# Kernel tuning notes

Measured on AMD Instinct MI355X. Metric: run time of the kernel, lower is better.

Reference implementation:

```python
import jax, jax.numpy as jnp
import numpy as np

# config constants
D = 1024       # main_dim
HD = 64        # attn_head_dim
NH = 16        # attention heads = D // HD
H = 16         # main_head_num (routing heads)
KH = 8         # main_key_head_num
KC = 2         # main_key_repeat_num (KH*KC == H)
N = 128        # block_size
E = 4096       # total_layer_expert_num
RE = 4         # aux_router_expert_num
DE = 4         # selected experts per router
ET = RE * DE   # 16
B, S = 1, 2048
T = B * S
BC = T // N    # 16
EPS = 1e-5
THETA = 10000.0


def rmsnorm(x, w):
    return x * jax.lax.rsqrt(jnp.mean(x * x, axis=-1, keepdims=True) + EPS) * w


def l2norm(x):
    n = jnp.sqrt(jnp.sum(x * x, axis=-1, keepdims=True))
    return x / jnp.maximum(n, EPS)


def rope(x):
    # x: (b, h, s, a); matches RotaryEmb: y1 = x1*cos + x2*sin, y2 = -x1*sin + x2*cos
    a = x.shape[-1]
    s = x.shape[2]
    inv_freq = (1.0 / THETA) ** (jnp.arange(0, a, 2, dtype=jnp.float32) / a)
    freqs = jnp.arange(s, dtype=jnp.float32)[:, None] * inv_freq[None, :]  # (s, a/2)
    cos, sin = jnp.cos(freqs), jnp.sin(freqs)
    x1, x2 = jnp.split(x, 2, axis=-1)
    return jnp.concatenate([x1 * cos + x2 * sin, -x1 * sin + x2 * cos], axis=-1)


def setup_inputs() -> dict:
    key = jax.random.key(0)
    ks = jax.random.split(key, 10)
    return {
        "x_input": jax.random.normal(ks[0], (B, S, D), jnp.float32),
        "indices": jax.random.randint(ks[1], (BC, RE, DE), 0, E),
        "scores": jax.random.normal(ks[2], (T, ET, H), jnp.float32),
        "attn_w": jax.random.normal(ks[3], (D, 3 * D), jnp.float32) * 0.02,
        "attn_out_w": jax.random.normal(ks[4], (D, D), jnp.float32) * 0.02,
        "attn_norm_w": jnp.ones((D,), jnp.float32),
        "ffn_norm_w": jnp.ones((D,), jnp.float32),
        "ffn_experts": jax.random.normal(ks[5], (3, E, D, 1), jnp.float32) * 0.02,
        "keys": jax.random.normal(ks[6], (KH, D, E), jnp.float32) * 0.02,
        "head_probs": jnp.full((1, RE, E, H), 1.0 / H, jnp.float32)
                      + 0.01 * jax.random.normal(ks[7], (1, RE, E, H), jnp.float32),
        "score_probs": jnp.full((2, 1, RE, E, H), 0.5, jnp.float32)
                       + 0.01 * jax.random.normal(ks[8], (2, 1, RE, E, H), jnp.float32),
    }


def reference(x_input, indices, scores, attn_w, attn_out_w, attn_norm_w,
              ffn_norm_w, ffn_experts, keys, head_probs, score_probs):
    # --- attention block ---
    x = rmsnorm(x_input, attn_norm_w)
    qkv = x @ attn_w                                   # (b, s, 3d)
    xq, xk, xv = jnp.split(qkv, 3, axis=-1)

    def heads(t):  # 'b s (h a) -> b h s a'
        return t.reshape(B, S, NH, HD).transpose(0, 2, 1, 3)

    xq, xk, xv = heads(xq), heads(xk), heads(xv)
    xq, xk = l2norm(xq), l2norm(xk)                    # qk_norm
    xq, xk = rope(xq), rope(xk)

    att = jnp.einsum('bhqa,bhka->bhqk', xq, xk) / np.sqrt(HD)
    causal = jnp.tril(jnp.ones((S, S), bool))
    att = jnp.where(causal, att, -jnp.inf)
    att = jax.nn.softmax(att, axis=-1)
    x_attn = jnp.einsum('bhqk,bhka->bhqa', att, xv)
    x_attn = x_attn.transpose(0, 2, 1, 3).reshape(B, S, D)
    x_attn_output = x_attn @ attn_out_w
    x_ffn_input = x_attn_output + x_input

    # --- product-key routing ---
    x_ffn = rmsnorm(x_ffn_input, ffn_norm_w)
    xf = x_ffn.reshape(T, D)

    keys_r = jnp.repeat(keys, KC, axis=0)              # (H, D, E)
    ms = jnp.einsum('td,hde->teh', xf, keys_r)         # (T, E, H)

    idx_flat = indices.reshape(BC, ET)                 # (BC, ET)
    idx_tok = jnp.repeat(idx_flat, N, axis=0)          # (T, ET), token t -> block t//N
    main_g = jnp.take_along_axis(ms, idx_tok[:, :, None], axis=1)  # (T, ET, H)

    r_idx = jnp.arange(RE)[None, :, None]
    sp = score_probs[:, 0]                             # (2, RE, E, H)
    sp_g = sp[:, r_idx, indices]                       # (2, BC, RE, DE, H)
    sp_g = jnp.repeat(sp_g.reshape(2, BC, ET, H), N, axis=1)       # (2, T, ET, H)

    comb = jax.nn.sigmoid(sp_g[0] * main_g + sp_g[1] * scores)     # (T, ET, H)

    hp_g = head_probs[0][r_idx, indices]               # (BC, RE, DE, H)
    hp_g = jnp.repeat(hp_g.reshape(BC, ET, H), N, axis=0)          # (T, ET, H)

    w = jnp.sum(comb * hp_g, axis=-1)                  # (T, ET) pair weights

    # --- grouped GEMM over tiny (d -> expert_dim -> d) experts, SwiGLU ---
    Wg = ffn_experts[:, idx_tok]                       # (3, T, ET, D, expert_dim)
    h0 = jnp.einsum('td,tedk->tek', xf, Wg[0])
    h1 = jnp.einsum('td,tedk->tek', xf, Wg[1])
    act = jax.nn.silu(h0) * h1 * w[:, :, None]         # (T, ET, expert_dim)
    out = jnp.einsum('tek,tedk->td', act, Wg[2])       # sum over selected experts

    return out.reshape(B, S, D) + x_ffn_input
```

## Files before the change

### kernel.cpp

```cpp
#include <hip/hip_runtime.h>
#include <hip/hip_bf16.h>
#include <math.h>

#define D_   1024
#define HD_  64
#define NH_  16
#define H_   16
#define KH_  8
#define NT_  128
#define E_   4096
#define RE_  4
#define DE_  4
#define ET_  16
#define S_   2048
#define T_   2048
#define BC_  16
#define EPS_ 1e-5f

typedef short s16x8 __attribute__((ext_vector_type(8)));
typedef float f32x4 __attribute__((ext_vector_type(4)));

__device__ __forceinline__ unsigned short f2bf(float f) {
    union { float f; unsigned int u; } v; v.f = f;
    unsigned int r = (v.u + 0x7fffu + ((v.u >> 16) & 1u)) >> 16;
    return (unsigned short)r;
}

#define GLOAD16(gp, lp) __builtin_amdgcn_global_load_lds(                      \
    (__attribute__((address_space(1))) void*)(gp),                             \
    (__attribute__((address_space(3))) void*)(lp), 16, 0, 0)

__global__ __launch_bounds__(256) void preprocess_kernel(
    const float* __restrict__ x, const float* __restrict__ attn_norm_w,
    unsigned short* __restrict__ xnb,
    const float* __restrict__ attn_w, unsigned short* __restrict__ wqkvT,
    const float* __restrict__ attn_out_w, unsigned short* __restrict__ woutT,
    const float* __restrict__ keys, const int* __restrict__ indices,
    unsigned short* __restrict__ tmpT)
{
    __shared__ float tile[32][33];
    __shared__ float sred[4];
    __shared__ float rowbuf[E_];
    int bid = blockIdx.x, tid = threadIdx.x;

    if (bid < 2048) {
        int row = bid;
        float4 v = ((const float4*)(x + (size_t)row * D_))[tid];
        float ss = v.x*v.x + v.y*v.y + v.z*v.z + v.w*v.w;
#pragma unroll
        for (int off = 32; off > 0; off >>= 1) ss += __shfl_xor(ss, off);
        if ((tid & 63) == 0) sred[tid >> 6] = ss;
        __syncthreads();
        float tot = sred[0] + sred[1] + sred[2] + sred[3];
        float scale = rsqrtf(tot * (1.0f / D_) + EPS_);
        float4 wv = ((const float4*)attn_norm_w)[tid];
        ushort4 o;
        o.x = f2bf(v.x * scale * wv.x);
        o.y = f2bf(v.y * scale * wv.y);
        o.z = f2bf(v.z * scale * wv.z);
        o.w = f2bf(v.w * scale * wv.w);
        *(ushort4*)(xnb + (size_t)row * D_ + tid * 4) = o;
    } else if (bid < 6144) {
        const float* src; unsigned short* dst; int R, Ncols, bx, by;
        if (bid < 5120) {
            int cid = bid - 2048;
            src = attn_w; dst = wqkvT; R = D_; Ncols = 3 * D_;
            bx = (cid % 96) * 32; by = (cid / 96) * 32;
        } else {
            int cid = bid - 5120;
            src = attn_out_w; dst = woutT; R = D_; Ncols = D_;
            bx = (cid & 31) * 32; by = (cid >> 5) * 32;
        }
        int tx = tid & 31, ty = tid >> 5;
#pragma unroll
        for (int rr = 0; rr < 32; rr += 8)
            tile[ty + rr][tx] = src[(size_t)(by + ty + rr) * Ncols + bx + tx];
        __syncthreads();
#pragma unroll
        for (int rr = 0; rr < 32; rr += 8)
            dst[(size_t)(bx + ty + rr) * R + by + tx] = f2bf(tile[tx][ty + rr]);
    } else {
        int id = bid - 6144;
        int kh = id >> 10;
        int d  = id & (D_ - 1);
        const float* rowp = keys + ((size_t)kh * D_ + d) * E_;
#pragma unroll
        for (int pass = 0; pass < 4; pass++)
            ((float4*)rowbuf)[tid + pass * 256] =
                ((const float4*)rowp)[tid + pass * 256];
        __syncthreads();
        int idx = indices[tid];
        tmpT[((size_t)kh * D_ + d) * 256 + tid] = f2bf(rowbuf[idx]);
    }
}

__global__ __launch_bounds__(256) void transpose_keys_kernel(
    const unsigned short* __restrict__ tmpT, unsigned short* __restrict__ kgath)
{
    __shared__ unsigned short tile[32][34];
    int p0 = blockIdx.x * 32;
    int d0 = blockIdx.y * 32;
    int kh = blockIdx.z;
    int tx = threadIdx.x & 31, ty = threadIdx.x >> 5;
#pragma unroll
    for (int rr = 0; rr < 32; rr += 8)
        tile[ty + rr][tx] = tmpT[((size_t)kh * D_ + d0 + ty + rr) * 256 + p0 + tx];
    __syncthreads();
#pragma unroll
    for (int rr = 0; rr < 32; rr += 8) {
        int p = p0 + ty + rr;
        int n = (p >> 4) * 128 + (p & 15) * 8 + kh;
        kgath[(size_t)n * D_ + d0 + tx] = tile[tx][ty + rr];
    }
}

__global__ __launch_bounds__(256) void rmsnorm_dual_kernel(
    const float* __restrict__ x, const float* __restrict__ w,
    float* __restrict__ out, unsigned short* __restrict__ outb)
{
    int row = blockIdx.x, tid = threadIdx.x;
    __shared__ float sred[4];
    float4 v = ((const float4*)(x + (size_t)row * D_))[tid];
    float ss = v.x*v.x + v.y*v.y + v.z*v.z + v.w*v.w;
#pragma unroll
    for (int off = 32; off > 0; off >>= 1) ss += __shfl_xor(ss, off);
    if ((tid & 63) == 0) sred[tid >> 6] = ss;
    __syncthreads();
    float tot = sred[0] + sred[1] + sred[2] + sred[3];
    float scale = rsqrtf(tot * (1.0f / D_) + EPS_);
    float4 wv = ((const float4*)w)[tid];
    float4 o;
    o.x = v.x * scale * wv.x;
    o.y = v.y * scale * wv.y;
    o.z = v.z * scale * wv.z;
    o.w = v.w * scale * wv.w;
    ((float4*)(out + (size_t)row * D_))[tid] = o;
    ushort4 ob;
    ob.x = f2bf(o.x); ob.y = f2bf(o.y); ob.z = f2bf(o.z); ob.w = f2bf(o.w);
    *(ushort4*)(outb + (size_t)row * D_ + tid * 4) = ob;
}

template <int WITH_RES>
__global__ __launch_bounds__(256) void mfma_gemm_kernel(
    const unsigned short* __restrict__ A, const unsigned short* __restrict__ Bt,
    const float* __restrict__ res, float* __restrict__ C,
    int M, int N, int K)
{
    __shared__ __align__(16) short As[128][32];
    __shared__ __align__(16) short Bs[128][32];
    int tid = threadIdx.x;
    int wave = tid >> 6, lane = tid & 63;
    int ml = lane & 15, q = lane >> 4;
    int wr = wave >> 1, wc = wave & 1;
    int bm = blockIdx.y * 128, bn = blockIdx.x * 128;
    int srow = tid >> 2;
    int scol = (tid & 3) * 8;

    f32x4 acc[4][4];
#pragma unroll
    for (int i = 0; i < 4; i++)
#pragma unroll
        for (int j = 0; j < 4; j++) acc[i][j] = (f32x4){0.f, 0.f, 0.f, 0.f};

    const unsigned short* Ap = A  + (size_t)(bm + srow) * K + scol;
    const unsigned short* Bp = Bt + (size_t)(bn + srow) * K + scol;
    short* ldsA0 = &As[wave * 16][0];
    short* ldsA1 = &As[64 + wave * 16][0];
    short* ldsB0 = &Bs[wave * 16][0];
    short* ldsB1 = &Bs[64 + wave * 16][0];

    for (int k0 = 0; k0 < K; k0 += 32) {
        __syncthreads();
        GLOAD16(Ap + k0, ldsA0);
        GLOAD16(Ap + (size_t)64 * K + k0, ldsA1);
        GLOAD16(Bp + k0, ldsB0);
        GLOAD16(Bp + (size_t)64 * K + k0, ldsB1);
        __syncthreads();

        s16x8 af[4], bf[4];
#pragma unroll
        for (int i = 0; i < 4; i++)
            af[i] = *(const s16x8*)(&As[wr * 64 + i * 16 + ml][q * 8]);
#pragma unroll
        for (int j = 0; j < 4; j++)
            bf[j] = *(const s16x8*)(&Bs[wc * 64 + j * 16 + ml][q * 8]);
#pragma unroll
        for (int i = 0; i < 4; i++)
#pragma unroll
            for (int j = 0; j < 4; j++)
                acc[i][j] = __builtin_amdgcn_mfma_f32_16x16x32_bf16(
                    af[i], bf[j], acc[i][j], 0, 0, 0);
    }

#pragma unroll
    for (int i = 0; i < 4; i++) {
#pragma unroll
        for (int j = 0; j < 4; j++) {
            int col = bn + wc * 64 + j * 16 + ml;
#pragma unroll
            for (int r = 0; r < 4; r++) {
                int row = bm + wr * 64 + i * 16 + q * 4 + r;
                float v = acc[i][j][r];
                if (WITH_RES) v += res[(size_t)row * N + col];
                C[(size_t)row * N + col] = v;
            }
        }
    }
}

__global__ __launch_bounds__(256) void mfma_gemm_qkv_kernel(
    const unsigned short* __restrict__ A, const unsigned short* __restrict__ Bt,
    unsigned short* __restrict__ qh, unsigned short* __restrict__ khb,
    unsigned short* __restrict__ vhT)
{
    const int K = D_;
    __shared__ __align__(16) short As[128][32];
    __shared__ __align__(16) short Bs[128][32];
    int tid = threadIdx.x;
    int wave = tid >> 6, lane = tid & 63;
    int ml = lane & 15, q = lane >> 4;
    int wr = wave >> 1, wc = wave & 1;
    int bm = blockIdx.y * 128, bn = blockIdx.x * 128;
    int srow = tid >> 2;
    int scol = (tid & 3) * 8;

    f32x4 acc[4][4];
#pragma unroll
    for (int i = 0; i < 4; i++)
#pragma unroll
        for (int j = 0; j < 4; j++) acc[i][j] = (f32x4){0.f, 0.f, 0.f, 0.f};

    const unsigned short* Ap = A  + (size_t)(bm + srow) * K + scol;
    const unsigned short* Bp = Bt + (size_t)(bn + srow) * K + scol;
    short* ldsA0 = &As[wave * 16][0];
    short* ldsA1 = &As[64 + wave * 16][0];
    short* ldsB0 = &Bs[wave * 16][0];
    short* ldsB1 = &Bs[64 + wave * 16][0];

    for (int k0 = 0; k0 < K; k0 += 32) {
        __syncthreads();
        GLOAD16(Ap + k0, ldsA0);
        GLOAD16(Ap + (size_t)64 * K + k0, ldsA1);
        GLOAD16(Bp + k0, ldsB0);
        GLOAD16(Bp + (size_t)64 * K + k0, ldsB1);
        __syncthreads();

        s16x8 af[4], bf[4];
#pragma unroll
        for (int i = 0; i < 4; i++)
            af[i] = *(const s16x8*)(&As[wr * 64 + i * 16 + ml][q * 8]);
#pragma unroll
        for (int j = 0; j < 4; j++)
            bf[j] = *(const s16x8*)(&Bs[wc * 64 + j * 16 + ml][q * 8]);
#pragma unroll
        for (int i = 0; i < 4; i++)
#pragma unroll
            for (int j = 0; j < 4; j++)
                acc[i][j] = __builtin_amdgcn_mfma_f32_16x16x32_bf16(
                    af[i], bf[j], acc[i][j], 0, 0, 0);
    }

    int sel = blockIdx.x >> 3;
    int h = ((blockIdx.x & 7) << 1) + wc;
    float qscale = (sel == 0) ? 0.125f : 1.0f;
    float if0 = exp2f((float)ml * (-13.287712379549449f / 32.0f));
    float if1 = exp2f((float)(16 + ml) * (-13.287712379549449f / 32.0f));

#pragma unroll
    for (int i = 0; i < 4; i++) {
#pragma unroll
        for (int r = 0; r < 4; r++) {
            int row = bm + wr * 64 + i * 16 + q * 4 + r;
            float v0 = acc[i][0][r], v1 = acc[i][1][r];
            float v2 = acc[i][2][r], v3 = acc[i][3][r];
            if (sel < 2) {
                float ss = v0*v0 + v1*v1 + v2*v2 + v3*v3;
#pragma unroll
                for (int off = 1; off < 16; off <<= 1)
                    ss += __shfl_xor(ss, off);
                float inv = qscale / fmaxf(sqrtf(ss), EPS_);
                v0 *= inv; v1 *= inv; v2 *= inv; v3 *= inv;
                float sn0, cs0, sn1, cs1;
                sincosf((float)row * if0, &sn0, &cs0);
                sincosf((float)row * if1, &sn1, &cs1);
                float o0 = v0 * cs0 + v2 * sn0;
                float o2 = v2 * cs0 - v0 * sn0;
                float o1 = v1 * cs1 + v3 * sn1;
                float o3 = v3 * cs1 - v1 * sn1;
                v0 = o0; v1 = o1; v2 = o2; v3 = o3;
                unsigned short* dst = (sel == 0) ? qh : khb;
                size_t base = ((size_t)h * S_ + row) * HD_;
                dst[base +      ml] = f2bf(v0);
                dst[base + 16 + ml] = f2bf(v1);
                dst[base + 32 + ml] = f2bf(v2);
                dst[base + 48 + ml] = f2bf(v3);
            } else {
                size_t base = ((size_t)h * HD_ + ml) * S_ + row;
                vhT[base            ] = f2bf(v0);
                vhT[base + 16 * S_  ] = f2bf(v1);
                vhT[base + 32 * S_  ] = f2bf(v2);
                vhT[base + 48 * S_  ] = f2bf(v3);
            }
        }
    }
}

#define FS 72
__global__ __launch_bounds__(256) void flash_attn_mfma_kernel(
    const unsigned short* __restrict__ qh, const unsigned short* __restrict__ khb,
    const unsigned short* __restrict__ vhT, unsigned short* __restrict__ aob)
{
    __shared__ __align__(16) short Ks[2][64][FS];
    __shared__ __align__(16) short Vs[2][64][FS];
    __shared__ __align__(16) short Ps[4][16][FS];
    int b = blockIdx.x;
    int xcd = b & 7, j = b >> 3;
    int h = 2 * xcd + (j & 1);
    int pp = (j >> 1) & 15;
    int t = (j >> 5) ? (31 - pp) : pp;
    int tid = threadIdx.x;
    int wq = tid >> 6;
    int lane = tid & 63;
    int ml = lane & 15, quad = lane >> 4;
    int srow = tid >> 2;
    int sc = (tid & 3) * 16;
    const unsigned short* Qb = qh  + (size_t)h * S_ * HD_;
    const unsigned short* Kb = khb + (size_t)h * S_ * HD_;
    const unsigned short* Vt = vhT + (size_t)h * HD_ * S_;

    int q0 = t * 64;
    int qrow = q0 + wq * 16 + ml;
    s16x8 aq0 = *(const s16x8*)(Qb + (size_t)qrow * HD_ + quad * 8);
    s16x8 aq1 = *(const s16x8*)(Qb + (size_t)qrow * HD_ + 32 + quad * 8);

    float ps[4];
    f32x4 o[4];
#pragma unroll
    for (int r = 0; r < 4; r++) ps[r] = 0.f;
#pragma unroll
    for (int nb = 0; nb < 4; nb++) o[nb] = (f32x4){0.f, 0.f, 0.f, 0.f};

    int4 kr0, kr1, vr0, vr1;
    {
        const unsigned short* kp = Kb + (size_t)srow * HD_ + sc;
        kr0 = *(const int4*)kp; kr1 = *(const int4*)(kp + 8);
        const unsigned short* vp = Vt + (size_t)srow * S_ + sc;
        vr0 = *(const int4*)vp; vr1 = *(const int4*)(vp + 8);
        *(int4*)(&Ks[0][srow][sc]) = kr0; *(int4*)(&Ks[0][srow][sc + 8]) = kr1;
        *(int4*)(&Vs[0][srow][sc]) = vr0; *(int4*)(&Vs[0][srow][sc + 8]) = vr1;
    }

    for (int kt = 0; kt <= t; kt++) {
        int k0 = kt * 64;
        int cur = kt & 1;
        if (kt < t) {
            const unsigned short* kp = Kb + (size_t)(k0 + 64 + srow) * HD_ + sc;
            kr0 = *(const int4*)kp; kr1 = *(const int4*)(kp + 8);
            const unsigned short* vp = Vt + (size_t)srow * S_ + k0 + 64 + sc;
            vr0 = *(const int4*)vp; vr1 = *(const int4*)(vp + 8);
        }
        __syncthreads();

        f32x4 s[4];
#pragma unroll
        for (int nb = 0; nb < 4; nb++) s[nb] = (f32x4){0.f, 0.f, 0.f, 0.f};
        __builtin_amdgcn_s_setprio(1);
#pragma unroll
        for (int nb = 0; nb < 4; nb++) {
            s16x8 b0 = *(const s16x8*)(&Ks[cur][nb * 16 + ml][quad * 8]);
            s16x8 b1 = *(const s16x8*)(&Ks[cur][nb * 16 + ml][32 + quad * 8]);
            s[nb] = __builtin_amdgcn_mfma_f32_16x16x32_bf16(aq0, b0, s[nb], 0, 0, 0);
            s[nb] = __builtin_amdgcn_mfma_f32_16x16x32_bf16(aq1, b1, s[nb], 0, 0, 0);
        }
        __builtin_amdgcn_s_setprio(0);

#pragma unroll
        for (int nb = 0; nb < 4; nb++)
#pragma unroll
            for (int r = 0; r < 4; r++) {
                float pe = __expf(s[nb][r]);
                if (kt == t && (nb * 16 + ml) > (wq * 16 + quad * 4 + r))
                    pe = 0.f;
                ps[r] += pe;
                Ps[wq][quad * 4 + r][nb * 16 + ml] = (short)f2bf(pe);
            }

        s16x8 ap0 = *(const s16x8*)(&Ps[wq][ml][quad * 8]);
        s16x8 ap1 = *(const s16x8*)(&Ps[wq][ml][32 + quad * 8]);
        __builtin_amdgcn_s_setprio(1);
#pragma unroll
        for (int nb = 0; nb < 4; nb++) {
            s16x8 b0 = *(const s16x8*)(&Vs[cur][nb * 16 + ml][quad * 8]);
            s16x8 b1 = *(const s16x8*)(&Vs[cur][nb * 16 + ml][32 + quad * 8]);
            o[nb] = __builtin_amdgcn_mfma_f32_16x16x32_bf16(ap0, b0, o[nb], 0, 0, 0);
            o[nb] = __builtin_amdgcn_mfma_f32_16x16x32_bf16(ap1, b1, o[nb], 0, 0, 0);
        }
        __builtin_amdgcn_s_setprio(0);

        if (kt < t) {
            *(int4*)(&Ks[cur ^ 1][srow][sc])     = kr0;
            *(int4*)(&Ks[cur ^ 1][srow][sc + 8]) = kr1;
            *(int4*)(&Vs[cur ^ 1][srow][sc])     = vr0;
            *(int4*)(&Vs[cur ^ 1][srow][sc + 8]) = vr1;
        }
    }

#pragma unroll
    for (int r = 0; r < 4; r++) {
        float l = ps[r];
#pragma unroll
        for (int off = 1; off < 16; off <<= 1)
            l += __shfl_xor(l, off);
        float inv = 1.0f / l;
        int row = q0 + wq * 16 + quad * 4 + r;
#pragma unroll
        for (int nb = 0; nb < 4; nb++)
            aob[(size_t)row * D_ + h * HD_ + nb * 16 + ml] =
                f2bf(o[nb][r] * inv);
    }
}

__global__ __launch_bounds__(256) void score_gemm_kernel(
    const unsigned short* __restrict__ xfb, const unsigned short* __restrict__ kgath,
    float* __restrict__ msbufp)
{
    __shared__ __align__(16) short As[128][32];
    __shared__ __align__(16) short Bs[128][32];
    int c  = blockIdx.x >> 3;
    int sk = blockIdx.x & 7;
    const unsigned short* A  = xfb   + (size_t)c * 128 * D_ + sk * 128;
    const unsigned short* Bt = kgath + (size_t)c * 128 * D_ + sk * 128;
    int tid = threadIdx.x;
    int wave = tid >> 6, lane = tid & 63;
    int ml = lane & 15, q = lane >> 4;
    int wr = wave >> 1, wc = wave & 1;
    int srow = tid >> 2;
    int scol = (tid & 3) * 8;

    f32x4 acc[4][4];
#pragma unroll
    for (int i = 0; i < 4; i++)
#pragma unroll
        for (int j = 0; j < 4; j++) acc[i][j] = (f32x4){0.f, 0.f, 0.f, 0.f};

    const unsigned short* Ap = A  + (size_t)srow * D_ + scol;
    const unsigned short* Bp = Bt + (size_t)srow * D_ + scol;
    short* ldsA0 = &As[wave * 16][0];
    short* ldsA1 = &As[64 + wave * 16][0];
    short* ldsB0 = &Bs[wave * 16][0];
    short* ldsB1 = &Bs[64 + wave * 16][0];

    for (int k0 = 0; k0 < 128; k0 += 32) {
        __syncthreads();
        GLOAD16(Ap + k0, ldsA0);
        GLOAD16(Ap + (size_t)64 * D_ + k0, ldsA1);
        GLOAD16(Bp + k0, ldsB0);
        GLOAD16(Bp + (size_t)64 * D_ + k0, ldsB1);
        __syncthreads();

        s16x8 af[4], bf[4];
#pragma unroll
        for (int i = 0; i < 4; i++)
            af[i] = *(const s16x8*)(&As[wr * 64 + i * 16 + ml][q * 8]);
#pragma unroll
        for (int j = 0; j < 4; j++)
            bf[j] = *(const s16x8*)(&Bs[wc * 64 + j * 16 + ml][q * 8]);
#pragma unroll
        for (int i = 0; i < 4; i++)
#pragma unroll
            for (int j = 0; j < 4; j++)
                acc[i][j] = __builtin_amdgcn_mfma_f32_16x16x32_bf16(
                    af[i], bf[j], acc[i][j], 0, 0, 0);
    }

    float* out = msbufp + (size_t)blockIdx.x * 128 * 128;
#pragma unroll
    for (int i = 0; i < 4; i++)
#pragma unroll
        for (int j = 0; j < 4; j++) {
            int col = wc * 64 + j * 16 + ml;
#pragma unroll
            for (int r = 0; r < 4; r++) {
                int row = wr * 64 + i * 16 + q * 4 + r;
                out[(size_t)row * 128 + col] = acc[i][j][r];
            }
        }
}

__global__ __launch_bounds__(256) void moe_kernel(
    const float* __restrict__ xf, const float* __restrict__ xfi,
    const int* __restrict__ indices, const float* __restrict__ msbufp,
    const float* __restrict__ scores,
    const float* __restrict__ score_probs, const float* __restrict__ head_probs,
    const float* __restrict__ experts, float* __restrict__ out)
{
    int g = blockIdx.x, tid = threadIdx.x;
    int c = g >> 5;
    int t0 = c * NT_ + (g & 31) * 4;
    __shared__ int sidx[ET_];
    __shared__ float sw[4][ET_];
    __shared__ float sact[4][ET_];
    __shared__ float sx[4][D_];
    if (tid < ET_) sidx[tid] = indices[c * ET_ + tid];
#pragma unroll
    for (int tt = 0; tt < 4; tt++)
        ((float4*)sx[tt])[tid] =
            ((const float4*)(xf + (size_t)(t0 + tt) * D_))[tid];
    {
        int e = tid >> 4, hh = tid & 15;
        int idxe = indices[c * ET_ + e];
        int rr = e >> 2;
        float sp0 = score_probs[((size_t)rr * E_ + idxe) * H_ + hh];
        float sp1 = score_probs[((size_t)(RE_ + rr) * E_ + idxe) * H_ + hh];
        float hp  = head_probs[((size_t)rr * E_ + idxe) * H_ + hh];
#pragma unroll
        for (int tt = 0; tt < 4; tt++) {
            int t = t0 + tt;
            int trow = t & 127;
            const float* mp = msbufp + ((size_t)(c * 8) * 128 + trow) * 128
                                     + e * 8 + (hh >> 1);
            float ms = 0.f;
#pragma unroll
            for (int sck = 0; sck < 8; sck++)
                ms += mp[(size_t)sck * 128 * 128];
            float scv = scores[(size_t)t * (ET_ * H_) + tid];
            float z = sp0 * ms + sp1 * scv;
            float term = hp / (1.0f + __expf(-z));
#pragma unroll
            for (int off = 1; off < 16; off <<= 1)
                term += __shfl_xor(term, off);
            if (hh == 0) sw[tt][e] = term;
        }
    }
    __syncthreads();

    int wv = tid >> 6, lane = tid & 63;
#pragma unroll
    for (int ee = 0; ee < 4; ee++) {
        int e = wv * 4 + ee;
        int idx = sidx[e];
        size_t base = (size_t)idx * D_;
        float p0[4] = {0.f, 0.f, 0.f, 0.f};
        float p1[4] = {0.f, 0.f, 0.f, 0.f};
#pragma unroll
        for (int rr = 0; rr < 4; rr++) {
            int dd = rr * 256 + lane * 4;
            float4 w0 = *(const float4*)(experts + base + dd);
            float4 w1 = *(const float4*)(experts + (size_t)E_ * D_ + base + dd);
#pragma unroll
            for (int tt = 0; tt < 4; tt++) {
                float4 xr = *(const float4*)(&sx[tt][dd]);
                p0[tt] += xr.x*w0.x + xr.y*w0.y + xr.z*w0.z + xr.w*w0.w;
                p1[tt] += xr.x*w1.x + xr.y*w1.y + xr.z*w1.z + xr.w*w1.w;
            }
        }
#pragma unroll
        for (int tt = 0; tt < 4; tt++) {
#pragma unroll
            for (int off = 32; off > 0; off >>= 1) {
                p0[tt] += __shfl_xor(p0[tt], off);
                p1[tt] += __shfl_xor(p1[tt], off);
            }
        }
        if (lane == 0) {
#pragma unroll
            for (int tt = 0; tt < 4; tt++)
                sact[tt][e] = p0[tt] / (1.0f + __expf(-p0[tt])) * p1[tt]
                              * sw[tt][e];
        }
    }
    __syncthreads();

    float4 a0 = {0,0,0,0}, a1 = {0,0,0,0}, a2 = {0,0,0,0}, a3 = {0,0,0,0};
    const float* w2base = experts + (size_t)2 * E_ * D_;
#pragma unroll
    for (int e = 0; e < ET_; e++) {
        float4 w2 = *(const float4*)(w2base + (size_t)sidx[e] * D_ + tid * 4);
        float c0 = sact[0][e], c1 = sact[1][e], c2 = sact[2][e], c3 = sact[3][e];
        a0.x += c0 * w2.x; a0.y += c0 * w2.y; a0.z += c0 * w2.z; a0.w += c0 * w2.w;
        a1.x += c1 * w2.x; a1.y += c1 * w2.y; a1.z += c1 * w2.z; a1.w += c1 * w2.w;
        a2.x += c2 * w2.x; a2.y += c2 * w2.y; a2.z += c2 * w2.z; a2.w += c2 * w2.w;
        a3.x += c3 * w2.x; a3.y += c3 * w2.y; a3.z += c3 * w2.z; a3.w += c3 * w2.w;
    }
#pragma unroll
    for (int tt = 0; tt < 4; tt++) {
        float4 av = (tt == 0) ? a0 : (tt == 1) ? a1 : (tt == 2) ? a2 : a3;
        size_t o = (size_t)(t0 + tt) * D_ + tid * 4;
        float4 rv = *(const float4*)(xfi + o);
        float4 ov;
        ov.x = av.x + rv.x;
        ov.y = av.y + rv.y;
        ov.z = av.z + rv.z;
        ov.w = av.w + rv.w;
        *(float4*)(out + o) = ov;
    }
}

extern "C" void kernel_launch(void* const* d_in, const int* in_sizes, int n_in,
                              void* d_out, int out_size, void* d_ws, size_t ws_size,
                              hipStream_t stream)
{
    (void)in_sizes; (void)n_in; (void)out_size; (void)ws_size;
    const float* x_input     = (const float*)d_in[0];
    const int*   indices     = (const int*)d_in[1];
    const float* scores      = (const float*)d_in[2];
    const float* attn_w      = (const float*)d_in[3];
    const float* attn_out_w  = (const float*)d_in[4];
    const float* attn_norm_w = (const float*)d_in[5];
    const float* ffn_norm_w  = (const float*)d_in[6];
    const float* ffn_experts = (const float*)d_in[7];
    const float* keys        = (const float*)d_in[8];
    const float* head_probs  = (const float*)d_in[9];
    const float* score_probs = (const float*)d_in[10];
    float* out = (float*)d_out;

    float* ws = (float*)d_ws;
    const size_t MF = 1024 * 1024;
    unsigned short* qh    = (unsigned short*)ws;
    unsigned short* khb   = (unsigned short*)(ws + 1 * MF);
    unsigned short* tmpT  = (unsigned short*)(ws + 2 * MF);
    unsigned short* vhT   = (unsigned short*)(ws + 3 * MF);
    float* xfi            = ws + 4 * MF;
    unsigned short* xnb   = (unsigned short*)(ws + 6 * MF);
    unsigned short* aob   = (unsigned short*)(ws + 6 * MF);
    unsigned short* woutT = (unsigned short*)(ws + 7 * MF);
    unsigned short* wqkvT = (unsigned short*)(ws + 8 * MF);
    float* xf             = ws + 8 * MF;
    unsigned short* kgath = (unsigned short*)(ws + 10 * MF);
    unsigned short* xfb   = (unsigned short*)(ws + 11 * MF);
    float* msbufp         = ws + 12 * MF;

    preprocess_kernel<<<14336, 256, 0, stream>>>(
        x_input, attn_norm_w, xnb, attn_w, wqkvT, attn_out_w, woutT,
        keys, indices, tmpT);

    {
        dim3 g(256 / 32, D_ / 32, KH_);
        transpose_keys_kernel<<<g, 256, 0, stream>>>(tmpT, kgath);
    }

    {
        dim3 g(3 * D_ / 128, T_ / 128);
        mfma_gemm_qkv_kernel<<<g, 256, 0, stream>>>(xnb, wqkvT, qh, khb, vhT);
    }

    flash_attn_mfma_kernel<<<(S_ / 64) * NH_, 256, 0, stream>>>(qh, khb, vhT, aob);

    {
        dim3 g(D_ / 128, T_ / 128);
        mfma_gemm_kernel<1><<<g, 256, 0, stream>>>(aob, woutT, x_input, xfi,
                                                   T_, D_, D_);
    }

    rmsnorm_dual_kernel<<<T_, 256, 0, stream>>>(xfi, ffn_norm_w, xf, xfb);

    score_gemm_kernel<<<BC_ * 8, 256, 0, stream>>>(xfb, kgath, msbufp);

    moe_kernel<<<T_ / 4, 256, 0, stream>>>(xf, xfi, indices, msbufp, scores,
                                           score_probs, head_probs,
                                           ffn_experts, out);
}
```

Baseline: 372.4 us.

## Split causal flash attention KV range across two blocks and combine partials

Each query tile's key/value tiles are now split by parity into two halves, so twice as many blocks run flash attention. Each block writes unnormalized fp32 partial outputs and row sums, and a new combine kernel adds the two halves, normalizes and writes bf16. This raises parallelism and shortens the longest per-block causal loop. In exchange it adds an extra launch and an fp32 round trip of partials through global memory. The split relies on the kernel using no running max, so the two partials can be summed directly.

Result: no change. 379.4 us (+1.9%).

```diff
diff --git a/kernel.cpp b/kernel.cpp
--- a/kernel.cpp
+++ b/kernel.cpp
@@ -308,7 +308,8 @@
 #define FS 72
 __global__ __launch_bounds__(256) void flash_attn_mfma_kernel(
     const unsigned short* __restrict__ qh, const unsigned short* __restrict__ khb,
-    const unsigned short* __restrict__ vhT, unsigned short* __restrict__ aob)
+    const unsigned short* __restrict__ vhT,
+    float* __restrict__ opart, float* __restrict__ lpart)
 {
     __shared__ __align__(16) short Ks[2][64][FS];
     __shared__ __align__(16) short Vs[2][64][FS];
@@ -316,8 +317,9 @@
     int b = blockIdx.x;
     int xcd = b & 7, j = b >> 3;
     int h = 2 * xcd + (j & 1);
-    int pp = (j >> 1) & 15;
-    int t = (j >> 5) ? (31 - pp) : pp;
+    int j2 = j >> 1;
+    int pp = j2 & 31, half = j2 >> 5;
+    int t = (pp < 16) ? pp : (47 - pp);
     int tid = threadIdx.x;
     int wq = tid >> 6;
     int lane = tid & 63;
@@ -342,21 +344,21 @@
 
     int4 kr0, kr1, vr0, vr1;
     {
-        const unsigned short* kp = Kb + (size_t)srow * HD_ + sc;
+        const unsigned short* kp = Kb + (size_t)(half * 64 + srow) * HD_ + sc;
         kr0 = *(const int4*)kp; kr1 = *(const int4*)(kp + 8);
-        const unsigned short* vp = Vt + (size_t)srow * S_ + sc;
+        const unsigned short* vp = Vt + (size_t)srow * S_ + half * 64 + sc;
         vr0 = *(const int4*)vp; vr1 = *(const int4*)(vp + 8);
         *(int4*)(&Ks[0][srow][sc]) = kr0; *(int4*)(&Ks[0][srow][sc + 8]) = kr1;
         *(int4*)(&Vs[0][srow][sc]) = vr0; *(int4*)(&Vs[0][srow][sc + 8]) = vr1;
     }
 
-    for (int kt = 0; kt <= t; kt++) {
+    int cur = 0;
+    for (int kt = half; kt <= t; kt += 2) {
         int k0 = kt * 64;
-        int cur = kt & 1;
-        if (kt < t) {
-            const unsigned short* kp = Kb + (size_t)(k0 + 64 + srow) * HD_ + sc;
+        if (kt + 2 <= t) {
+            const unsigned short* kp = Kb + (size_t)(k0 + 128 + srow) * HD_ + sc;
             kr0 = *(const int4*)kp; kr1 = *(const int4*)(kp + 8);
-            const unsigned short* vp = Vt + (size_t)srow * S_ + k0 + 64 + sc;
+            const unsigned short* vp = Vt + (size_t)srow * S_ + k0 + 128 + sc;
             vr0 = *(const int4*)vp; vr1 = *(const int4*)(vp + 8);
         }
         __syncthreads();
@@ -397,12 +399,13 @@
         }
         __builtin_amdgcn_s_setprio(0);
 
-        if (kt < t) {
+        if (kt + 2 <= t) {
             *(int4*)(&Ks[cur ^ 1][srow][sc])     = kr0;
             *(int4*)(&Ks[cur ^ 1][srow][sc + 8]) = kr1;
             *(int4*)(&Vs[cur ^ 1][srow][sc])     = vr0;
             *(int4*)(&Vs[cur ^ 1][srow][sc + 8]) = vr1;
         }
+        cur ^= 1;
     }
 
 #pragma unroll
@@ -411,13 +414,29 @@
 #pragma unroll
         for (int off = 1; off < 16; off <<= 1)
             l += __shfl_xor(l, off);
-        float inv = 1.0f / l;
         int row = q0 + wq * 16 + quad * 4 + r;
+        size_t rb = ((size_t)(half * NH_ + h) * S_ + row) * HD_;
 #pragma unroll
         for (int nb = 0; nb < 4; nb++)
-            aob[(size_t)row * D_ + h * HD_ + nb * 16 + ml] =
-                f2bf(o[nb][r] * inv);
-    }
+            opart[rb + nb * 16 + ml] = o[nb][r];
+        if (ml == 0)
+            lpart[(size_t)(half * NH_ + h) * S_ + row] = l;
+    }
+}
+
+__global__ __launch_bounds__(256) void flash_combine_kernel(
+    const float* __restrict__ opart, const float* __restrict__ lpart,
+    unsigned short* __restrict__ aob)
+{
+    int hs = blockIdx.x * 4 + (threadIdx.x >> 6);
+    int d = threadIdx.x & 63;
+    int h = hs >> 11;
+    int s = hs & (S_ - 1);
+    size_t i0 = (size_t)hs * HD_ + d;
+    size_t i1 = (size_t)(NH_ * S_ + hs) * HD_ + d;
+    float l = lpart[hs] + lpart[NH_ * S_ + hs];
+    float val = (opart[i0] + opart[i1]) / l;
+    aob[((size_t)s * NH_ + h) * HD_ + d] = f2bf(val);
 }
 
 __global__ __launch_bounds__(256) void score_gemm_kernel(
@@ -629,6 +648,8 @@
     unsigned short* kgath = (unsigned short*)(ws + 10 * MF);
     unsigned short* xfb   = (unsigned short*)(ws + 11 * MF);
     float* msbufp         = ws + 12 * MF;
+    float* opart          = ws + 14 * MF;
+    float* lpart          = ws + 18 * MF;
 
     preprocess_kernel<<<14336, 256, 0, stream>>>(
         x_input, attn_norm_w, xnb, attn_w, wqkvT, attn_out_w, woutT,
@@ -644,7 +665,10 @@
         mfma_gemm_qkv_kernel<<<g, 256, 0, stream>>>(xnb, wqkvT, qh, khb, vhT);
     }
 
-    flash_attn_mfma_kernel<<<(S_ / 64) * NH_, 256, 0, stream>>>(qh, khb, vhT, aob);
+    flash_attn_mfma_kernel<<<2 * (S_ / 64) * NH_, 256, 0, stream>>>(
+        qh, khb, vhT, opart, lpart);
+
+    flash_combine_kernel<<<NH_ * S_ / 4, 256, 0, stream>>>(opart, lpart, aob);
 
     {
         dim3 g(D_ / 128, T_ / 128);
```
